# Kernel optimization log

Hardware: AMD Instinct MI355X
Metric: run time of the kernel (lower is better)

## Reference

```python
import jax, jax.numpy as jnp
import numpy as np

B, N, D = 256, 50, 128
N_NODE, MAX_ATTR = 50000, 2000
ALPHA = 0.2  # LeakyReLU negative slope
STDV = 1.0 / np.sqrt(D)  # reset_parameters uniform(-stdv, stdv)
NEG = -9e15


def setup_inputs() -> dict:
    key = jax.random.key(0)
    ks = jax.random.split(key, 10)
    uni = lambda k, shp: jax.random.uniform(k, shp, jnp.float32, -STDV, STDV)
    return {
        "inputs": jax.random.randint(ks[0], (B, N), 0, N_NODE),
        "adj": jax.random.randint(ks[1], (B, N, N), 0, 5),
        "mask_item": jax.random.randint(ks[2], (B, N), 0, 2),
        "A_attr_sess": jax.random.normal(ks[3], (B, MAX_ATTR), jnp.float32),
        "embedding": uni(ks[4], (N_NODE, D)),
        "attr_embedding": uni(ks[5], (MAX_ATTR, D)),
        "a0": uni(ks[6], (D,)),
        "a1": uni(ks[7], (D,)),
        "a2": uni(ks[8], (D,)),
        "a3": uni(ks[9], (D,)),
    }


def reference(inputs, adj, mask_item, A_attr_sess, embedding, attr_embedding, a0, a1, a2, a3):
    h = embedding[inputs]  # [B, N, D]
    # (h.repeat(1,1,N) * h.repeat(1,N,1)).view(B,N,N,D) == outer elementwise product h_i * h_j
    a_in = jax.nn.leaky_relu(h[:, :, None, :] * h[:, None, :, :], ALPHA)  # [B,N,N,D]
    a_all = jnp.stack([a0, a1, a2, a3], axis=-1)  # [D, 4]
    e = jnp.einsum('bijd,dk->bijk', a_in, a_all)  # [B,N,N,4]
    alpha = jnp.full(adj.shape, NEG, dtype=e.dtype)
    alpha = jnp.where(adj == 1, e[..., 0], alpha)
    alpha = jnp.where(adj == 2, e[..., 1], alpha)
    alpha = jnp.where(adj == 3, e[..., 2], alpha)
    alpha = jnp.where(adj == 4, e[..., 3], alpha)
    alpha = jax.nn.softmax(alpha, axis=-1)
    output = jnp.einsum('bij,bjd->bid', alpha, h)  # [B, N, D]
    attr_sess = A_attr_sess @ attr_embedding  # [B, D]
    return output, attr_sess
```

## Files before the change

### kernel.cpp

```cpp
#include <hip/hip_runtime.h>
#include <math.h>

#define BB 256
#define NN 50
#define DD 128
#define MAXA 2000
#define NEGV -9e15f
#define NATTR 256
#define NRED 32

#define H_S   136
#define HT_S  72
#define AL_S  72

#define H_OFF   0
#define HT_OFF  (64 * H_S)
#define AL_OFF  (HT_OFF + 128 * HT_S)
#define ADJ_OFF (AL_OFF + 64 * AL_S)
#define LDS_US  (ADJ_OFF + 64 * 64)

typedef __attribute__((ext_vector_type(8))) short        s8b;
typedef __attribute__((ext_vector_type(4))) float        f32x4;
typedef __attribute__((ext_vector_type(4))) unsigned int u32x4;

static __device__ __forceinline__ unsigned int pack2(float lo, float hi) {
    unsigned int r;
    asm("v_cvt_pk_bf16_f32 %0, %1, %2" : "=v"(r) : "v"(lo), "v"(hi));
    return r;
}
static __device__ __forceinline__ float bf2f(unsigned int s) {
    return __uint_as_float(s << 16);
}
static __device__ __forceinline__ f32x4 mfma16(u32x4 a, u32x4 b, f32x4 c) {
    return __builtin_amdgcn_mfma_f32_16x16x32_bf16(
        __builtin_bit_cast(s8b, a), __builtin_bit_cast(s8b, b), c, 0, 0, 0);
}

__global__ __launch_bounds__(256) void attr_part_kernel(
    const float* __restrict__ A_attr,
    const float* __restrict__ attr_emb,
    float* __restrict__ ws)
{
    const int ablk = blockIdx.x;
    const int tid  = threadIdx.x;
    const int w    = tid >> 6;
    const int lane = tid & 63;
    const int g    = lane >> 4;
    const int c    = lane & 15;
    const int goff = g * 8;

    const int mg = ablk >> 4;
    const int ks = ablk & 15;
    const int m0 = mg * 16;
    const int wd = w * 32;
    const float* Arow = A_attr + (size_t)(m0 + c) * MAXA;

    f32x4 acc2[2];
    acc2[0] = (f32x4){0.f, 0.f, 0.f, 0.f};
    acc2[1] = (f32x4){0.f, 0.f, 0.f, 0.f};

    auto do_chunk = [&](int k0, bool guard) {
        float4 aL = make_float4(0.f, 0.f, 0.f, 0.f);
        float4 aH = make_float4(0.f, 0.f, 0.f, 0.f);
        if (!guard || k0 + goff + 3 < MAXA) aL = *(const float4*)(Arow + k0 + goff);
        if (!guard || k0 + goff + 7 < MAXA) aH = *(const float4*)(Arow + k0 + goff + 4);
        u32x4 af;
        af[0] = pack2(aL.x, aL.y); af[1] = pack2(aL.z, aL.w);
        af[2] = pack2(aH.x, aH.y); af[3] = pack2(aH.z, aH.w);
        #pragma unroll
        for (int ntl = 0; ntl < 2; ++ntl) {
            const int col = wd + ntl * 16 + c;
            float ev[8];
            #pragma unroll
            for (int p = 0; p < 8; ++p) {
                const int kr = k0 + goff + p;
                ev[p] = (!guard || kr < MAXA) ? attr_emb[(size_t)kr * DD + col] : 0.f;
            }
            u32x4 bf_;
            bf_[0] = pack2(ev[0], ev[1]); bf_[1] = pack2(ev[2], ev[3]);
            bf_[2] = pack2(ev[4], ev[5]); bf_[3] = pack2(ev[6], ev[7]);
            acc2[ntl] = mfma16(af, bf_, acc2[ntl]);
        }
    };
    #pragma unroll
    for (int q = 0; q < 3; ++q) do_chunk((ks + q * 16) * 32, false);
    if (ks + 48 < 63) do_chunk((ks + 48) * 32, (ks + 48) == 62);

    float* pt = ws + (size_t)ablk * (16 * DD);
    #pragma unroll
    for (int ntl = 0; ntl < 2; ++ntl)
        #pragma unroll
        for (int reg = 0; reg < 4; ++reg)
            pt[(g * 4 + reg) * DD + wd + ntl * 16 + c] = acc2[ntl][reg];
}

__global__ __launch_bounds__(256) void sg_gat_kernel(
    const int* __restrict__ inputs,
    const int* __restrict__ adj,
    const float* __restrict__ embedding,
    const float* __restrict__ a0,
    const float* __restrict__ a1,
    const float* __restrict__ a2,
    const float* __restrict__ a3,
    const float* __restrict__ ws,
    float* __restrict__ out,
    float* __restrict__ attr_out)
{
    __shared__ __align__(16) unsigned short sh[LDS_US];
    const int blk  = blockIdx.x;
    const int tid  = threadIdx.x;

    if (blk < NRED) {
        const int idx = blk * 256 + tid;
        const int m  = idx >> 5;
        const int d4 = idx & 31;
        const int mg = m >> 4;
        const int r  = m & 15;
        const float4* base = (const float4*)ws + (size_t)(mg * 16) * 512 + r * 32 + d4;
        float4 v = make_float4(0.f, 0.f, 0.f, 0.f);
        #pragma unroll
        for (int ks = 0; ks < 16; ++ks) {
            const float4 t = base[(size_t)ks * 512];
            v.x += t.x; v.y += t.y; v.z += t.z; v.w += t.w;
        }
        ((float4*)attr_out)[(size_t)m * 32 + d4] = v;
        return;
    }

    const int b    = blk - NRED;
    const int w    = tid >> 6;
    const int lane = tid & 63;
    const int g    = lane >> 4;
    const int c    = lane & 15;
    const int goff = g * 8;

    const int  i_   = lane;
    const bool live = (i_ < NN);
    int node = 0;
    if (live) node = inputs[b * NN + i_];
    float4 gv[8];
    #pragma unroll
    for (int n = 0; n < 8; ++n) {
        gv[n] = make_float4(0.f, 0.f, 0.f, 0.f);
        if (live) gv[n] = *(const float4*)(embedding + (size_t)node * DD + (w * 8 + n) * 4);
    }
    for (int idx = tid; idx < 4096; idx += 256) {
        const int i = idx >> 6, j = idx & 63;
        int a = 0;
        if (i < NN && j < NN) a = adj[(size_t)b * (NN * NN) + i * NN + j];
        sh[ADJ_OFF + idx] = (unsigned short)a;
    }
    #pragma unroll
    for (int n = 0; n < 8; ++n) {
        const int d4 = w * 8 + n;
        const unsigned int pk01 = pack2(gv[n].x, gv[n].y);
        const unsigned int pk23 = pack2(gv[n].z, gv[n].w);
        *(uint2*)(sh + H_OFF + i_ * H_S + d4 * 4) = make_uint2(pk01, pk23);
        sh[HT_OFF + (d4 * 4 + 0) * HT_S + i_] = (unsigned short)pk01;
        sh[HT_OFF + (d4 * 4 + 1) * HT_S + i_] = (unsigned short)(pk01 >> 16);
        sh[HT_OFF + (d4 * 4 + 2) * HT_S + i_] = (unsigned short)pk23;
        sh[HT_OFF + (d4 * 4 + 3) * HT_S + i_] = (unsigned short)(pk23 >> 16);
    }
    __syncthreads();

    u32x4 hA[4];
    #pragma unroll
    for (int dt = 0; dt < 4; ++dt)
        hA[dt] = *(const u32x4*)(const void*)(sh + H_OFF + (w * 16 + c) * H_S + dt * 32 + goff);

    f32x4 accS[4][4];
    #pragma unroll
    for (int jt = 0; jt < 4; ++jt)
        #pragma unroll
        for (int k = 0; k < 4; ++k) accS[jt][k] = (f32x4){0.f, 0.f, 0.f, 0.f};

    #pragma unroll
    for (int dt = 0; dt < 4; ++dt) {
        float hf8[8], hb8[8];
        #pragma unroll
        for (int p = 0; p < 4; ++p) {
            const unsigned int hp = hA[dt][p];
            hf8[2 * p]     = bf2f(hp & 0xffffu);
            hf8[2 * p + 1] = bf2f(hp >> 16);
            hb8[2 * p]     = fabsf(hf8[2 * p]);
            hb8[2 * p + 1] = fabsf(hf8[2 * p + 1]);
        }
        u32x4 U[4], V[4];
        #pragma unroll
        for (int k = 0; k < 4; ++k) {
            const float* ap = (k == 0) ? a0 : (k == 1) ? a1 : (k == 2) ? a2 : a3;
            const float4 aL = *(const float4*)(ap + dt * 32 + goff);
            const float4 aH = *(const float4*)(ap + dt * 32 + goff + 4);
            const float a8[8] = {aL.x, aL.y, aL.z, aL.w, aH.x, aH.y, aH.z, aH.w};
            #pragma unroll
            for (int p = 0; p < 4; ++p) {
                U[k][p] = pack2(0.6f * a8[2 * p] * hf8[2 * p],
                                0.6f * a8[2 * p + 1] * hf8[2 * p + 1]);
                V[k][p] = pack2(0.4f * a8[2 * p] * hb8[2 * p],
                                0.4f * a8[2 * p + 1] * hb8[2 * p + 1]);
            }
        }
        #pragma unroll
        for (int jt = 0; jt < 4; ++jt) {
            const u32x4 hB = *(const u32x4*)(const void*)(sh + H_OFF + (jt * 16 + c) * H_S + dt * 32 + goff);
            u32x4 hBa;
            #pragma unroll
            for (int p = 0; p < 4; ++p) hBa[p] = hB[p] & 0x7fff7fffu;
            #pragma unroll
            for (int k = 0; k < 4; ++k) {
                accS[jt][k] = mfma16(U[k], hB,  accS[jt][k]);
                accS[jt][k] = mfma16(V[k], hBa, accS[jt][k]);
            }
        }
    }

    float s_[4][4];
    #pragma unroll
    for (int jt = 0; jt < 4; ++jt) {
        #pragma unroll
        for (int reg = 0; reg < 4; ++reg) {
            const int il = w * 16 + g * 4 + reg;
            const int j  = jt * 16 + c;
            const int a  = (int)sh[ADJ_OFF + il * 64 + j];
            float sv = (a == 1) ? accS[jt][0][reg] : (a == 2) ? accS[jt][1][reg]
                     : (a == 3) ? accS[jt][2][reg] : (a == 4) ? accS[jt][3][reg] : NEGV;
            if (j >= NN) sv = -INFINITY;
            s_[jt][reg] = sv;
        }
    }
    #pragma unroll
    for (int reg = 0; reg < 4; ++reg) {
        float m = fmaxf(fmaxf(s_[0][reg], s_[1][reg]), fmaxf(s_[2][reg], s_[3][reg]));
        m = fmaxf(m, __shfl_xor(m, 1));
        m = fmaxf(m, __shfl_xor(m, 2));
        m = fmaxf(m, __shfl_xor(m, 4));
        m = fmaxf(m, __shfl_xor(m, 8));
        const float p0 = __expf(s_[0][reg] - m);
        const float p1 = __expf(s_[1][reg] - m);
        const float p2 = __expf(s_[2][reg] - m);
        const float p3 = __expf(s_[3][reg] - m);
        float sum = (p0 + p1) + (p2 + p3);
        sum += __shfl_xor(sum, 1);
        sum += __shfl_xor(sum, 2);
        sum += __shfl_xor(sum, 4);
        sum += __shfl_xor(sum, 8);
        const float r  = 1.0f / sum;
        const int  il  = w * 16 + g * 4 + reg;
        sh[AL_OFF + il * AL_S +  0 + c] = (unsigned short)pack2(p0 * r, p0 * r);
        sh[AL_OFF + il * AL_S + 16 + c] = (unsigned short)pack2(p1 * r, p1 * r);
        sh[AL_OFF + il * AL_S + 32 + c] = (unsigned short)pack2(p2 * r, p2 * r);
        sh[AL_OFF + il * AL_S + 48 + c] = (unsigned short)pack2(p3 * r, p3 * r);
    }

    const int il = w * 16 + c;
    const u32x4 pa0 = *(const u32x4*)(const void*)(sh + AL_OFF + il * AL_S + goff);
    const u32x4 pa1 = *(const u32x4*)(const void*)(sh + AL_OFF + il * AL_S + 32 + goff);
    #pragma unroll
    for (int nt = 0; nt < 8; ++nt) {
        const u32x4 v0 = *(const u32x4*)(const void*)(sh + HT_OFF + (nt * 16 + c) * HT_S + goff);
        const u32x4 v1 = *(const u32x4*)(const void*)(sh + HT_OFF + (nt * 16 + c) * HT_S + 32 + goff);
        f32x4 accp = (f32x4){0.f, 0.f, 0.f, 0.f};
        accp = mfma16(pa0, v0, accp);
        accp = mfma16(pa1, v1, accp);
        #pragma unroll
        for (int reg = 0; reg < 4; ++reg) {
            const int ig = w * 16 + g * 4 + reg;
            if (ig < NN)
                out[((size_t)b * NN + ig) * DD + nt * 16 + c] = accp[reg];
        }
    }
}

extern "C" void kernel_launch(void* const* d_in, const int* in_sizes, int n_in,
                              void* d_out, int out_size, void* d_ws, size_t ws_size,
                              hipStream_t stream) {
    const int*   inputs    = (const int*)  d_in[0];
    const int*   adj       = (const int*)  d_in[1];
    const float* A_attr    = (const float*)d_in[3];
    const float* embedding = (const float*)d_in[4];
    const float* attr_emb  = (const float*)d_in[5];
    const float* a0        = (const float*)d_in[6];
    const float* a1        = (const float*)d_in[7];
    const float* a2        = (const float*)d_in[8];
    const float* a3        = (const float*)d_in[9];

    float* out      = (float*)d_out;
    float* attr_out = out + (size_t)BB * NN * DD;
    float* ws       = (float*)d_ws;

    attr_part_kernel<<<NATTR, 256, 0, stream>>>(A_attr, attr_emb, ws);
    sg_gat_kernel<<<NRED + BB, 256, 0, stream>>>(inputs, adj, embedding,
                                                 a0, a1, a2, a3, ws,
                                                 out, attr_out);
}
```

Measured before the change: 22.73 us.

## Fuse attribute GEMM into GAT kernel, drop split-K workspace reduction

Merges the separate attribute-matmul kernel and its split-K reduction into one launch. The first 32 blocks each compute a full-K 16x64 tile of A_attr @ attr_embedding with a software-pipelined double-buffered loop, and write the result directly to the output. This removes a kernel launch and the workspace write/read round trip. In exchange, the attribute work is serialized over 63 K-chunks on only 32 blocks, which may become the critical path.

```diff
diff --git a/kernel.cpp b/kernel.cpp
--- a/kernel.cpp
+++ b/kernel.cpp
@@ -6,8 +6,7 @@
 #define DD 128
 #define MAXA 2000
 #define NEGV -9e15f
-#define NATTR 256
-#define NRED 32
+#define NATTR 32
 
 #define H_S   136
 #define HT_S  72
@@ -36,12 +35,21 @@
         __builtin_bit_cast(s8b, a), __builtin_bit_cast(s8b, b), c, 0, 0, 0);
 }
 
-__global__ __launch_bounds__(256) void attr_part_kernel(
+__global__ __launch_bounds__(256) void sg_fused_kernel(
+    const int* __restrict__ inputs,
+    const int* __restrict__ adj,
     const float* __restrict__ A_attr,
+    const float* __restrict__ embedding,
     const float* __restrict__ attr_emb,
-    float* __restrict__ ws)
+    const float* __restrict__ a0,
+    const float* __restrict__ a1,
+    const float* __restrict__ a2,
+    const float* __restrict__ a3,
+    float* __restrict__ out,
+    float* __restrict__ attr_out)
 {
-    const int ablk = blockIdx.x;
+    __shared__ __align__(16) unsigned short sh[LDS_US];
+    const int blk  = blockIdx.x;
     const int tid  = threadIdx.x;
     const int w    = tid >> 6;
     const int lane = tid & 63;
@@ -49,90 +57,59 @@
     const int c    = lane & 15;
     const int goff = g * 8;
 
-    const int mg = ablk >> 4;
-    const int ks = ablk & 15;
-    const int m0 = mg * 16;
-    const int wd = w * 32;
-    const float* Arow = A_attr + (size_t)(m0 + c) * MAXA;
-
-    f32x4 acc2[2];
-    acc2[0] = (f32x4){0.f, 0.f, 0.f, 0.f};
-    acc2[1] = (f32x4){0.f, 0.f, 0.f, 0.f};
-
-    auto do_chunk = [&](int k0, bool guard) {
-        float4 aL = make_float4(0.f, 0.f, 0.f, 0.f);
-        float4 aH = make_float4(0.f, 0.f, 0.f, 0.f);
-        if (!guard || k0 + goff + 3 < MAXA) aL = *(const float4*)(Arow + k0 + goff);
-        if (!guard || k0 + goff + 7 < MAXA) aH = *(const float4*)(Arow + k0 + goff + 4);
-        u32x4 af;
-        af[0] = pack2(aL.x, aL.y); af[1] = pack2(aL.z, aL.w);
-        af[2] = pack2(aH.x, aH.y); af[3] = pack2(aH.z, aH.w);
-        #pragma unroll
-        for (int ntl = 0; ntl < 2; ++ntl) {
-            const int col = wd + ntl * 16 + c;
-            float ev[8];
-            #pragma unroll
-            for (int p = 0; p < 8; ++p) {
-                const int kr = k0 + goff + p;
-                ev[p] = (!guard || kr < MAXA) ? attr_emb[(size_t)kr * DD + col] : 0.f;
+    if (blk < NATTR) {
+        const int mg   = blk >> 1;
+        const int ch   = blk & 1;
+        const int m0   = mg * 16;
+        const int colb = ch * 64 + w * 16;
+        const float* Arow = A_attr + (size_t)(m0 + c) * MAXA;
+        const float* Ecol = attr_emb + colb + c;
+
+        f32x4 acc = (f32x4){0.f, 0.f, 0.f, 0.f};
+
+        float4 aLA, aHA, aLB, aHB;
+        float  evA[8], evB[8];
+
+        auto loadc = [&](int k0, bool tail, float4& aL, float4& aH, float (&ev)[8]) {
+            if (!tail || g < 2) {
+                aL = *(const float4*)(Arow + k0 + goff);
+                aH = *(const float4*)(Arow + k0 + goff + 4);
+                #pragma unroll
+                for (int p = 0; p < 8; ++p)
+                    ev[p] = Ecol[(size_t)(k0 + goff + p) * DD];
+            } else {
+                aL = make_float4(0.f, 0.f, 0.f, 0.f);
+                aH = make_float4(0.f, 0.f, 0.f, 0.f);
+                #pragma unroll
+                for (int p = 0; p < 8; ++p) ev[p] = 0.f;
             }
-            u32x4 bf_;
+        };
+        auto compute = [&](const float4& aL, const float4& aH, const float (&ev)[8]) {
+            u32x4 af, bf_;
+            af[0] = pack2(aL.x, aL.y); af[1] = pack2(aL.z, aL.w);
+            af[2] = pack2(aH.x, aH.y); af[3] = pack2(aH.z, aH.w);
             bf_[0] = pack2(ev[0], ev[1]); bf_[1] = pack2(ev[2], ev[3]);
             bf_[2] = pack2(ev[4], ev[5]); bf_[3] = pack2(ev[6], ev[7]);
-            acc2[ntl] = mfma16(af, bf_, acc2[ntl]);
-        }
-    };
-    #pragma unroll
-    for (int q = 0; q < 3; ++q) do_chunk((ks + q * 16) * 32, false);
-    if (ks + 48 < 63) do_chunk((ks + 48) * 32, (ks + 48) == 62);
-
-    float* pt = ws + (size_t)ablk * (16 * DD);
-    #pragma unroll
-    for (int ntl = 0; ntl < 2; ++ntl)
+            acc = mfma16(af, bf_, acc);
+        };
+
+        loadc(0, false, aLA, aHA, evA);
+        #pragma unroll
+        for (int t = 0; t < 31; ++t) {
+            loadc((2 * t + 1) * 32, false, aLB, aHB, evB);
+            compute(aLA, aHA, evA);
+            loadc((2 * t + 2) * 32, (2 * t + 2) == 62, aLA, aHA, evA);
+            compute(aLB, aHB, evB);
+        }
+        compute(aLA, aHA, evA);
+
         #pragma unroll
         for (int reg = 0; reg < 4; ++reg)
-            pt[(g * 4 + reg) * DD + wd + ntl * 16 + c] = acc2[ntl][reg];
-}
-
-__global__ __launch_bounds__(256) void sg_gat_kernel(
-    const int* __restrict__ inputs,
-    const int* __restrict__ adj,
-    const float* __restrict__ embedding,
-    const float* __restrict__ a0,
-    const float* __restrict__ a1,
-    const float* __restrict__ a2,
-    const float* __restrict__ a3,
-    const float* __restrict__ ws,
-    float* __restrict__ out,
-    float* __restrict__ attr_out)
-{
-    __shared__ __align__(16) unsigned short sh[LDS_US];
-    const int blk  = blockIdx.x;
-    const int tid  = threadIdx.x;
-
-    if (blk < NRED) {
-        const int idx = blk * 256 + tid;
-        const int m  = idx >> 5;
-        const int d4 = idx & 31;
-        const int mg = m >> 4;
-        const int r  = m & 15;
-        const float4* base = (const float4*)ws + (size_t)(mg * 16) * 512 + r * 32 + d4;
-        float4 v = make_float4(0.f, 0.f, 0.f, 0.f);
-        #pragma unroll
-        for (int ks = 0; ks < 16; ++ks) {
-            const float4 t = base[(size_t)ks * 512];
-            v.x += t.x; v.y += t.y; v.z += t.z; v.w += t.w;
-        }
-        ((float4*)attr_out)[(size_t)m * 32 + d4] = v;
+            attr_out[(size_t)(m0 + g * 4 + reg) * DD + colb + c] = acc[reg];
         return;
     }
 
-    const int b    = blk - NRED;
-    const int w    = tid >> 6;
-    const int lane = tid & 63;
-    const int g    = lane >> 4;
-    const int c    = lane & 15;
-    const int goff = g * 8;
+    const int b = blk - NATTR;
 
     const int  i_   = lane;
     const bool live = (i_ < NN);
@@ -286,10 +263,8 @@
 
     float* out      = (float*)d_out;
     float* attr_out = out + (size_t)BB * NN * DD;
-    float* ws       = (float*)d_ws;
-
-    attr_part_kernel<<<NATTR, 256, 0, stream>>>(A_attr, attr_emb, ws);
-    sg_gat_kernel<<<NRED + BB, 256, 0, stream>>>(inputs, adj, embedding,
-                                                 a0, a1, a2, a3, ws,
-                                                 out, attr_out);
-}
+
+    sg_fused_kernel<<<NATTR + BB, 256, 0, stream>>>(inputs, adj, A_attr, embedding,
+                                                    attr_emb, a0, a1, a2, a3,
+                                                    out, attr_out);
+}
```

New measurement: 53.30 us. +134.5%, slower.

## Fuse attr partial GEMM into GAT kernel grid and split reduction into tail kernel

Applied to the files above, without the earlier changes.

Moves the attribute partial-product blocks into the same grid as the per-session GAT blocks, so the two independent workloads run concurrently instead of the GAT kernel waiting on the attr kernel. The small cross-K reduction now runs as its own short kernel afterwards. The attr path also issues all four chunks' global loads up front rather than chunk by chunk, to expose more memory parallelism. In exchange, attr blocks now carry the GAT kernel's LDS allocation and register footprint, which can lower occupancy, and a tiny extra launch is still needed.

```diff
diff --git a/kernel.cpp b/kernel.cpp
--- a/kernel.cpp
+++ b/kernel.cpp
@@ -7,7 +7,6 @@
 #define MAXA 2000
 #define NEGV -9e15f
 #define NATTR 256
-#define NRED 32
 
 #define H_S   136
 #define HT_S  72
@@ -36,12 +35,21 @@
         __builtin_bit_cast(s8b, a), __builtin_bit_cast(s8b, b), c, 0, 0, 0);
 }
 
-__global__ __launch_bounds__(256) void attr_part_kernel(
+__global__ __launch_bounds__(256) void sg_fused_kernel(
+    const int* __restrict__ inputs,
+    const int* __restrict__ adj,
     const float* __restrict__ A_attr,
+    const float* __restrict__ embedding,
     const float* __restrict__ attr_emb,
+    const float* __restrict__ a0,
+    const float* __restrict__ a1,
+    const float* __restrict__ a2,
+    const float* __restrict__ a3,
+    float* __restrict__ out,
     float* __restrict__ ws)
 {
-    const int ablk = blockIdx.x;
+    __shared__ __align__(16) unsigned short sh[LDS_US];
+    const int blk  = blockIdx.x;
     const int tid  = threadIdx.x;
     const int w    = tid >> 6;
     const int lane = tid & 63;
@@ -49,226 +57,234 @@
     const int c    = lane & 15;
     const int goff = g * 8;
 
-    const int mg = ablk >> 4;
-    const int ks = ablk & 15;
-    const int m0 = mg * 16;
-    const int wd = w * 32;
-    const float* Arow = A_attr + (size_t)(m0 + c) * MAXA;
-
-    f32x4 acc2[2];
-    acc2[0] = (f32x4){0.f, 0.f, 0.f, 0.f};
-    acc2[1] = (f32x4){0.f, 0.f, 0.f, 0.f};
-
-    auto do_chunk = [&](int k0, bool guard) {
-        float4 aL = make_float4(0.f, 0.f, 0.f, 0.f);
-        float4 aH = make_float4(0.f, 0.f, 0.f, 0.f);
-        if (!guard || k0 + goff + 3 < MAXA) aL = *(const float4*)(Arow + k0 + goff);
-        if (!guard || k0 + goff + 7 < MAXA) aH = *(const float4*)(Arow + k0 + goff + 4);
-        u32x4 af;
-        af[0] = pack2(aL.x, aL.y); af[1] = pack2(aL.z, aL.w);
-        af[2] = pack2(aH.x, aH.y); af[3] = pack2(aH.z, aH.w);
+    if (blk < BB) {
+        const int b = blk;
+
+        const int  i_   = lane;
+        const bool live = (i_ < NN);
+        int node = 0;
+        if (live) node = inputs[b * NN + i_];
+        float4 gv[8];
+        #pragma unroll
+        for (int n = 0; n < 8; ++n) {
+            gv[n] = make_float4(0.f, 0.f, 0.f, 0.f);
+            if (live) gv[n] = *(const float4*)(embedding + (size_t)node * DD + (w * 8 + n) * 4);
+        }
+        for (int idx = tid; idx < 4096; idx += 256) {
+            const int i = idx >> 6, j = idx & 63;
+            int a = 0;
+            if (i < NN && j < NN) a = adj[(size_t)b * (NN * NN) + i * NN + j];
+            sh[ADJ_OFF + idx] = (unsigned short)a;
+        }
+        #pragma unroll
+        for (int n = 0; n < 8; ++n) {
+            const int d4 = w * 8 + n;
+            const unsigned int pk01 = pack2(gv[n].x, gv[n].y);
+            const unsigned int pk23 = pack2(gv[n].z, gv[n].w);
+            *(uint2*)(sh + H_OFF + i_ * H_S + d4 * 4) = make_uint2(pk01, pk23);
+            sh[HT_OFF + (d4 * 4 + 0) * HT_S + i_] = (unsigned short)pk01;
+            sh[HT_OFF + (d4 * 4 + 1) * HT_S + i_] = (unsigned short)(pk01 >> 16);
+            sh[HT_OFF + (d4 * 4 + 2) * HT_S + i_] = (unsigned short)pk23;
+            sh[HT_OFF + (d4 * 4 + 3) * HT_S + i_] = (unsigned short)(pk23 >> 16);
+        }
+        __syncthreads();
+
+        u32x4 hA[4];
+        #pragma unroll
+        for (int dt = 0; dt < 4; ++dt)
+            hA[dt] = *(const u32x4*)(const void*)(sh + H_OFF + (w * 16 + c) * H_S + dt * 32 + goff);
+
+        f32x4 accS[4][4];
+        #pragma unroll
+        for (int jt = 0; jt < 4; ++jt)
+            #pragma unroll
+            for (int k = 0; k < 4; ++k) accS[jt][k] = (f32x4){0.f, 0.f, 0.f, 0.f};
+
+        #pragma unroll
+        for (int dt = 0; dt < 4; ++dt) {
+            float hf8[8], hb8[8];
+            #pragma unroll
+            for (int p = 0; p < 4; ++p) {
+                const unsigned int hp = hA[dt][p];
+                hf8[2 * p]     = bf2f(hp & 0xffffu);
+                hf8[2 * p + 1] = bf2f(hp >> 16);
+                hb8[2 * p]     = fabsf(hf8[2 * p]);
+                hb8[2 * p + 1] = fabsf(hf8[2 * p + 1]);
+            }
+            u32x4 U[4], V[4];
+            #pragma unroll
+            for (int k = 0; k < 4; ++k) {
+                const float* ap = (k == 0) ? a0 : (k == 1) ? a1 : (k == 2) ? a2 : a3;
+                const float4 aL = *(const float4*)(ap + dt * 32 + goff);
+                const float4 aH = *(const float4*)(ap + dt * 32 + goff + 4);
+                const float a8[8] = {aL.x, aL.y, aL.z, aL.w, aH.x, aH.y, aH.z, aH.w};
+                #pragma unroll
+                for (int p = 0; p < 4; ++p) {
+                    U[k][p] = pack2(0.6f * a8[2 * p] * hf8[2 * p],
+                                    0.6f * a8[2 * p + 1] * hf8[2 * p + 1]);
+                    V[k][p] = pack2(0.4f * a8[2 * p] * hb8[2 * p],
+                                    0.4f * a8[2 * p + 1] * hb8[2 * p + 1]);
+                }
+            }
+            #pragma unroll
+            for (int jt = 0; jt < 4; ++jt) {
+                const u32x4 hB = *(const u32x4*)(const void*)(sh + H_OFF + (jt * 16 + c) * H_S + dt * 32 + goff);
+                u32x4 hBa;
+                #pragma unroll
+                for (int p = 0; p < 4; ++p) hBa[p] = hB[p] & 0x7fff7fffu;
+                #pragma unroll
+                for (int k = 0; k < 4; ++k) {
+                    accS[jt][k] = mfma16(U[k], hB,  accS[jt][k]);
+                    accS[jt][k] = mfma16(V[k], hBa, accS[jt][k]);
+                }
+            }
+        }
+
+        float s_[4][4];
+        #pragma unroll
+        for (int jt = 0; jt < 4; ++jt) {
+            #pragma unroll
+            for (int reg = 0; reg < 4; ++reg) {
+                const int il = w * 16 + g * 4 + reg;
+                const int j  = jt * 16 + c;
+                const int a  = (int)sh[ADJ_OFF + il * 64 + j];
+                float sv = (a == 1) ? accS[jt][0][reg] : (a == 2) ? accS[jt][1][reg]
+                         : (a == 3) ? accS[jt][2][reg] : (a == 4) ? accS[jt][3][reg] : NEGV;
+                if (j >= NN) sv = -INFINITY;
+                s_[jt][reg] = sv;
+            }
+        }
+        #pragma unroll
+        for (int reg = 0; reg < 4; ++reg) {
+            float m = fmaxf(fmaxf(s_[0][reg], s_[1][reg]), fmaxf(s_[2][reg], s_[3][reg]));
+            m = fmaxf(m, __shfl_xor(m, 1));
+            m = fmaxf(m, __shfl_xor(m, 2));
+            m = fmaxf(m, __shfl_xor(m, 4));
+            m = fmaxf(m, __shfl_xor(m, 8));
+            const float p0 = __expf(s_[0][reg] - m);
+            const float p1 = __expf(s_[1][reg] - m);
+            const float p2 = __expf(s_[2][reg] - m);
+            const float p3 = __expf(s_[3][reg] - m);
+            float sum = (p0 + p1) + (p2 + p3);
+            sum += __shfl_xor(sum, 1);
+            sum += __shfl_xor(sum, 2);
+            sum += __shfl_xor(sum, 4);
+            sum += __shfl_xor(sum, 8);
+            const float r  = 1.0f / sum;
+            const int  il  = w * 16 + g * 4 + reg;
+            sh[AL_OFF + il * AL_S +  0 + c] = (unsigned short)pack2(p0 * r, p0 * r);
+            sh[AL_OFF + il * AL_S + 16 + c] = (unsigned short)pack2(p1 * r, p1 * r);
+            sh[AL_OFF + il * AL_S + 32 + c] = (unsigned short)pack2(p2 * r, p2 * r);
+            sh[AL_OFF + il * AL_S + 48 + c] = (unsigned short)pack2(p3 * r, p3 * r);
+        }
+
+        const int il = w * 16 + c;
+        const u32x4 pa0 = *(const u32x4*)(const void*)(sh + AL_OFF + il * AL_S + goff);
+        const u32x4 pa1 = *(const u32x4*)(const void*)(sh + AL_OFF + il * AL_S + 32 + goff);
+        #pragma unroll
+        for (int nt = 0; nt < 8; ++nt) {
+            const u32x4 v0 = *(const u32x4*)(const void*)(sh + HT_OFF + (nt * 16 + c) * HT_S + goff);
+            const u32x4 v1 = *(const u32x4*)(const void*)(sh + HT_OFF + (nt * 16 + c) * HT_S + 32 + goff);
+            f32x4 accp = (f32x4){0.f, 0.f, 0.f, 0.f};
+            accp = mfma16(pa0, v0, accp);
+            accp = mfma16(pa1, v1, accp);
+            #pragma unroll
+            for (int reg = 0; reg < 4; ++reg) {
+                const int ig = w * 16 + g * 4 + reg;
+                if (ig < NN)
+                    out[((size_t)b * NN + ig) * DD + nt * 16 + c] = accp[reg];
+            }
+        }
+    } else {
+        const int ablk = blk - BB;
+        const int mg = ablk >> 4;
+        const int ks = ablk & 15;
+        const int m0 = mg * 16;
+        const int wd = w * 32;
+        const float* Arow = A_attr + (size_t)(m0 + c) * MAXA;
+
+        const int k0 = (ks +  0) * 32;
+        const int k1 = (ks + 16) * 32;
+        const int k2 = (ks + 32) * 32;
+        const int k3 = (ks + 48) * 32;
+        const bool has3 = (ks < 15);
+        const bool gd3  = (ks == 14);
+
+        const float4 aL0 = *(const float4*)(Arow + k0 + goff);
+        const float4 aH0 = *(const float4*)(Arow + k0 + goff + 4);
+        const float4 aL1 = *(const float4*)(Arow + k1 + goff);
+        const float4 aH1 = *(const float4*)(Arow + k1 + goff + 4);
+        const float4 aL2 = *(const float4*)(Arow + k2 + goff);
+        const float4 aH2 = *(const float4*)(Arow + k2 + goff + 4);
+        float4 aL3 = make_float4(0.f, 0.f, 0.f, 0.f);
+        float4 aH3 = make_float4(0.f, 0.f, 0.f, 0.f);
+        if (has3) {
+            if (!gd3 || k3 + goff + 3 < MAXA) aL3 = *(const float4*)(Arow + k3 + goff);
+            if (!gd3 || k3 + goff + 7 < MAXA) aH3 = *(const float4*)(Arow + k3 + goff + 4);
+        }
+        float ev0[2][8], ev1[2][8], ev2[2][8], ev3[2][8];
         #pragma unroll
         for (int ntl = 0; ntl < 2; ++ntl) {
             const int col = wd + ntl * 16 + c;
-            float ev[8];
             #pragma unroll
             for (int p = 0; p < 8; ++p) {
-                const int kr = k0 + goff + p;
-                ev[p] = (!guard || kr < MAXA) ? attr_emb[(size_t)kr * DD + col] : 0.f;
-            }
-            u32x4 bf_;
-            bf_[0] = pack2(ev[0], ev[1]); bf_[1] = pack2(ev[2], ev[3]);
-            bf_[2] = pack2(ev[4], ev[5]); bf_[3] = pack2(ev[6], ev[7]);
-            acc2[ntl] = mfma16(af, bf_, acc2[ntl]);
-        }
-    };
+                ev0[ntl][p] = attr_emb[(size_t)(k0 + goff + p) * DD + col];
+                ev1[ntl][p] = attr_emb[(size_t)(k1 + goff + p) * DD + col];
+                ev2[ntl][p] = attr_emb[(size_t)(k2 + goff + p) * DD + col];
+                const int kr = k3 + goff + p;
+                ev3[ntl][p] = (has3 && (!gd3 || kr < MAXA))
+                                  ? attr_emb[(size_t)kr * DD + col] : 0.f;
+            }
+        }
+        f32x4 acc2[2];
+        acc2[0] = (f32x4){0.f, 0.f, 0.f, 0.f};
+        acc2[1] = (f32x4){0.f, 0.f, 0.f, 0.f};
+        #define ATTR_CHUNK(AL, AH, EV)                                              \
+        {                                                                           \
+            u32x4 af;                                                               \
+            af[0] = pack2(AL.x, AL.y); af[1] = pack2(AL.z, AL.w);                   \
+            af[2] = pack2(AH.x, AH.y); af[3] = pack2(AH.z, AH.w);                   \
+            _Pragma("unroll")                                                       \
+            for (int ntl = 0; ntl < 2; ++ntl) {                                     \
+                u32x4 bf_;                                                          \
+                bf_[0] = pack2(EV[ntl][0], EV[ntl][1]);                             \
+                bf_[1] = pack2(EV[ntl][2], EV[ntl][3]);                             \
+                bf_[2] = pack2(EV[ntl][4], EV[ntl][5]);                             \
+                bf_[3] = pack2(EV[ntl][6], EV[ntl][7]);                             \
+                acc2[ntl] = mfma16(af, bf_, acc2[ntl]);                             \
+            }                                                                       \
+        }
+        ATTR_CHUNK(aL0, aH0, ev0)
+        ATTR_CHUNK(aL1, aH1, ev1)
+        ATTR_CHUNK(aL2, aH2, ev2)
+        ATTR_CHUNK(aL3, aH3, ev3)
+        #undef ATTR_CHUNK
+
+        float* pt = ws + (size_t)ablk * (16 * DD);
+        #pragma unroll
+        for (int ntl = 0; ntl < 2; ++ntl)
+            #pragma unroll
+            for (int reg = 0; reg < 4; ++reg)
+                pt[(g * 4 + reg) * DD + wd + ntl * 16 + c] = acc2[ntl][reg];
+    }
+}
+
+__global__ __launch_bounds__(256) void attr_reduce_kernel(
+    const float* __restrict__ ws, float* __restrict__ attr_out)
+{
+    const int idx = blockIdx.x * 256 + threadIdx.x;
+    const int m  = idx >> 5;
+    const int d4 = idx & 31;
+    const int mg = m >> 4;
+    const int r  = m & 15;
+    const float4* base = (const float4*)ws + (size_t)(mg * 16) * 512 + r * 32 + d4;
+    float4 v = make_float4(0.f, 0.f, 0.f, 0.f);
     #pragma unroll
-    for (int q = 0; q < 3; ++q) do_chunk((ks + q * 16) * 32, false);
-    if (ks + 48 < 63) do_chunk((ks + 48) * 32, (ks + 48) == 62);
-
-    float* pt = ws + (size_t)ablk * (16 * DD);
-    #pragma unroll
-    for (int ntl = 0; ntl < 2; ++ntl)
-        #pragma unroll
-        for (int reg = 0; reg < 4; ++reg)
-            pt[(g * 4 + reg) * DD + wd + ntl * 16 + c] = acc2[ntl][reg];
-}
-
-__global__ __launch_bounds__(256) void sg_gat_kernel(
-    const int* __restrict__ inputs,
-    const int* __restrict__ adj,
-    const float* __restrict__ embedding,
-    const float* __restrict__ a0,
-    const float* __restrict__ a1,
-    const float* __restrict__ a2,
-    const float* __restrict__ a3,
-    const float* __restrict__ ws,
-    float* __restrict__ out,
-    float* __restrict__ attr_out)
-{
-    __shared__ __align__(16) unsigned short sh[LDS_US];
-    const int blk  = blockIdx.x;
-    const int tid  = threadIdx.x;
-
-    if (blk < NRED) {
-        const int idx = blk * 256 + tid;
-        const int m  = idx >> 5;
-        const int d4 = idx & 31;
-        const int mg = m >> 4;
-        const int r  = m & 15;
-        const float4* base = (const float4*)ws + (size_t)(mg * 16) * 512 + r * 32 + d4;
-        float4 v = make_float4(0.f, 0.f, 0.f, 0.f);
-        #pragma unroll
-        for (int ks = 0; ks < 16; ++ks) {
-            const float4 t = base[(size_t)ks * 512];
-            v.x += t.x; v.y += t.y; v.z += t.z; v.w += t.w;
-        }
-        ((float4*)attr_out)[(size_t)m * 32 + d4] = v;
-        return;
+    for (int ks = 0; ks < 16; ++ks) {
+        const float4 t = base[(size_t)ks * 512];
+        v.x += t.x; v.y += t.y; v.z += t.z; v.w += t.w;
     }
-
-    const int b    = blk - NRED;
-    const int w    = tid >> 6;
-    const int lane = tid & 63;
-    const int g    = lane >> 4;
-    const int c    = lane & 15;
-    const int goff = g * 8;
-
-    const int  i_   = lane;
-    const bool live = (i_ < NN);
-    int node = 0;
-    if (live) node = inputs[b * NN + i_];
-    float4 gv[8];
-    #pragma unroll
-    for (int n = 0; n < 8; ++n) {
-        gv[n] = make_float4(0.f, 0.f, 0.f, 0.f);
-        if (live) gv[n] = *(const float4*)(embedding + (size_t)node * DD + (w * 8 + n) * 4);
-    }
-    for (int idx = tid; idx < 4096; idx += 256) {
-        const int i = idx >> 6, j = idx & 63;
-        int a = 0;
-        if (i < NN && j < NN) a = adj[(size_t)b * (NN * NN) + i * NN + j];
-        sh[ADJ_OFF + idx] = (unsigned short)a;
-    }
-    #pragma unroll
-    for (int n = 0; n < 8; ++n) {
-        const int d4 = w * 8 + n;
-        const unsigned int pk01 = pack2(gv[n].x, gv[n].y);
-        const unsigned int pk23 = pack2(gv[n].z, gv[n].w);
-        *(uint2*)(sh + H_OFF + i_ * H_S + d4 * 4) = make_uint2(pk01, pk23);
-        sh[HT_OFF + (d4 * 4 + 0) * HT_S + i_] = (unsigned short)pk01;
-        sh[HT_OFF + (d4 * 4 + 1) * HT_S + i_] = (unsigned short)(pk01 >> 16);
-        sh[HT_OFF + (d4 * 4 + 2) * HT_S + i_] = (unsigned short)pk23;
-        sh[HT_OFF + (d4 * 4 + 3) * HT_S + i_] = (unsigned short)(pk23 >> 16);
-    }
-    __syncthreads();
-
-    u32x4 hA[4];
-    #pragma unroll
-    for (int dt = 0; dt < 4; ++dt)
-        hA[dt] = *(const u32x4*)(const void*)(sh + H_OFF + (w * 16 + c) * H_S + dt * 32 + goff);
-
-    f32x4 accS[4][4];
-    #pragma unroll
-    for (int jt = 0; jt < 4; ++jt)
-        #pragma unroll
-        for (int k = 0; k < 4; ++k) accS[jt][k] = (f32x4){0.f, 0.f, 0.f, 0.f};
-
-    #pragma unroll
-    for (int dt = 0; dt < 4; ++dt) {
-        float hf8[8], hb8[8];
-        #pragma unroll
-        for (int p = 0; p < 4; ++p) {
-            const unsigned int hp = hA[dt][p];
-            hf8[2 * p]     = bf2f(hp & 0xffffu);
-            hf8[2 * p + 1] = bf2f(hp >> 16);
-            hb8[2 * p]     = fabsf(hf8[2 * p]);
-            hb8[2 * p + 1] = fabsf(hf8[2 * p + 1]);
-        }
-        u32x4 U[4], V[4];
-        #pragma unroll
-        for (int k = 0; k < 4; ++k) {
-            const float* ap = (k == 0) ? a0 : (k == 1) ? a1 : (k == 2) ? a2 : a3;
-            const float4 aL = *(const float4*)(ap + dt * 32 + goff);
-            const float4 aH = *(const float4*)(ap + dt * 32 + goff + 4);
-            const float a8[8] = {aL.x, aL.y, aL.z, aL.w, aH.x, aH.y, aH.z, aH.w};
-            #pragma unroll
-            for (int p = 0; p < 4; ++p) {
-                U[k][p] = pack2(0.6f * a8[2 * p] * hf8[2 * p],
-                                0.6f * a8[2 * p + 1] * hf8[2 * p + 1]);
-                V[k][p] = pack2(0.4f * a8[2 * p] * hb8[2 * p],
-                                0.4f * a8[2 * p + 1] * hb8[2 * p + 1]);
-            }
-        }
-        #pragma unroll
-        for (int jt = 0; jt < 4; ++jt) {
-            const u32x4 hB = *(const u32x4*)(const void*)(sh + H_OFF + (jt * 16 + c) * H_S + dt * 32 + goff);
-            u32x4 hBa;
-            #pragma unroll
-            for (int p = 0; p < 4; ++p) hBa[p] = hB[p] & 0x7fff7fffu;
-            #pragma unroll
-            for (int k = 0; k < 4; ++k) {
-                accS[jt][k] = mfma16(U[k], hB,  accS[jt][k]);
-                accS[jt][k] = mfma16(V[k], hBa, accS[jt][k]);
-            }
-        }
-    }
-
-    float s_[4][4];
-    #pragma unroll
-    for (int jt = 0; jt < 4; ++jt) {
-        #pragma unroll
-        for (int reg = 0; reg < 4; ++reg) {
-            const int il = w * 16 + g * 4 + reg;
-            const int j  = jt * 16 + c;
-            const int a  = (int)sh[ADJ_OFF + il * 64 + j];
-            float sv = (a == 1) ? accS[jt][0][reg] : (a == 2) ? accS[jt][1][reg]
-                     : (a == 3) ? accS[jt][2][reg] : (a == 4) ? accS[jt][3][reg] : NEGV;
-            if (j >= NN) sv = -INFINITY;
-            s_[jt][reg] = sv;
-        }
-    }
-    #pragma unroll
-    for (int reg = 0; reg < 4; ++reg) {
-        float m = fmaxf(fmaxf(s_[0][reg], s_[1][reg]), fmaxf(s_[2][reg], s_[3][reg]));
-        m = fmaxf(m, __shfl_xor(m, 1));
-        m = fmaxf(m, __shfl_xor(m, 2));
-        m = fmaxf(m, __shfl_xor(m, 4));
-        m = fmaxf(m, __shfl_xor(m, 8));
-        const float p0 = __expf(s_[0][reg] - m);
-        const float p1 = __expf(s_[1][reg] - m);
-        const float p2 = __expf(s_[2][reg] - m);
-        const float p3 = __expf(s_[3][reg] - m);
-        float sum = (p0 + p1) + (p2 + p3);
-        sum += __shfl_xor(sum, 1);
-        sum += __shfl_xor(sum, 2);
-        sum += __shfl_xor(sum, 4);
-        sum += __shfl_xor(sum, 8);
-        const float r  = 1.0f / sum;
-        const int  il  = w * 16 + g * 4 + reg;
-        sh[AL_OFF + il * AL_S +  0 + c] = (unsigned short)pack2(p0 * r, p0 * r);
-        sh[AL_OFF + il * AL_S + 16 + c] = (unsigned short)pack2(p1 * r, p1 * r);
-        sh[AL_OFF + il * AL_S + 32 + c] = (unsigned short)pack2(p2 * r, p2 * r);
-        sh[AL_OFF + il * AL_S + 48 + c] = (unsigned short)pack2(p3 * r, p3 * r);
-    }
-
-    const int il = w * 16 + c;
-    const u32x4 pa0 = *(const u32x4*)(const void*)(sh + AL_OFF + il * AL_S + goff);
-    const u32x4 pa1 = *(const u32x4*)(const void*)(sh + AL_OFF + il * AL_S + 32 + goff);
-    #pragma unroll
-    for (int nt = 0; nt < 8; ++nt) {
-        const u32x4 v0 = *(const u32x4*)(const void*)(sh + HT_OFF + (nt * 16 + c) * HT_S + goff);
-        const u32x4 v1 = *(const u32x4*)(const void*)(sh + HT_OFF + (nt * 16 + c) * HT_S + 32 + goff);
-        f32x4 accp = (f32x4){0.f, 0.f, 0.f, 0.f};
-        accp = mfma16(pa0, v0, accp);
-        accp = mfma16(pa1, v1, accp);
-        #pragma unroll
-        for (int reg = 0; reg < 4; ++reg) {
-            const int ig = w * 16 + g * 4 + reg;
-            if (ig < NN)
-                out[((size_t)b * NN + ig) * DD + nt * 16 + c] = accp[reg];
-        }
-    }
+    ((float4*)attr_out)[(size_t)m * 32 + d4] = v;
 }
 
 extern "C" void kernel_launch(void* const* d_in, const int* in_sizes, int n_in,
@@ -288,8 +304,8 @@
     float* attr_out = out + (size_t)BB * NN * DD;
     float* ws       = (float*)d_ws;
 
-    attr_part_kernel<<<NATTR, 256, 0, stream>>>(A_attr, attr_emb, ws);
-    sg_gat_kernel<<<NRED + BB, 256, 0, stream>>>(inputs, adj, embedding,
-                                                 a0, a1, a2, a3, ws,
-                                                 out, attr_out);
-}
+    sg_fused_kernel<<<BB + NATTR, 256, 0, stream>>>(inputs, adj, A_attr, embedding,
+                                                    attr_emb, a0, a1, a2, a3,
+                                                    out, ws);
+    attr_reduce_kernel<<<32, 256, 0, stream>>>(ws, attr_out);
+}
```

Measured after the change: 20.50 us. 9.8% less time.
